# Kernel optimization log

Measured on AMD Instinct MI355X. Metric: run time of the kernel, lower is better.

Reference implementation:

```python
import jax, jax.numpy as jnp
import numpy as np
import math

# Hardcoded model constants (from source globals)
N_LAYERS = 4
MAX_SEQ_LEN = 34
VOCAB_SIZE = 14
TOK_DIM = 3
POS_DIM = 3
D_MODEL = 6
HEAD_DIM = 3
N_POS = 10
MAX_DIGITS = 10
ANSWER_LEN = 11
X_START, PLUS_POS, Y_START, EQ_POS, Z_START, EOS_POS = 0, 10, 11, 21, 22, 33
PLUS_TOKEN, EQUALS_TOKEN, EOS_TOKEN, PAD_TOKEN = 10, 11, 12, 13
BATCH = 16384


def _spiral(i, p):
    return (math.cos(2 * math.pi * i / p), math.sin(2 * math.pi * i / p), i / max(p - 1, 1))


def _build_pos_enc():
    pe = np.zeros((MAX_SEQ_LEN, POS_DIM), np.float32)
    for i in range(MAX_DIGITS):
        pe[X_START + i] = _spiral(i, N_POS)
    for i in range(MAX_DIGITS):
        pe[Y_START + i] = _spiral(i, N_POS)
    for i in range(min(ANSWER_LEN, N_POS)):
        pe[Z_START + i] = _spiral(i, N_POS)
    pe[Z_START + 10] = [0.0, 0.0, 1.5]
    pe[PLUS_POS] = [2.0, 0.0, -1.0]
    pe[EQ_POS] = [0.0, 2.0, -1.0]
    pe[EOS_POS] = [-2.0, 0.0, -1.0]
    return jnp.asarray(pe)


def _build_tok_emb():
    emb = np.zeros((VOCAB_SIZE, TOK_DIM), np.float32)
    for d in range(10):
        emb[d] = _spiral(d, 10)
    emb[PLUS_TOKEN] = [2.0, 0.0, -1.0]
    emb[EQUALS_TOKEN] = [0.0, 2.0, -1.0]
    emb[EOS_TOKEN] = [-2.0, 0.0, -1.0]
    emb[PAD_TOKEN] = [0.0, -2.0, -1.0]
    return jnp.asarray(emb)


def _xavier(key, shape):
    fan_out, fan_in = shape[-2], shape[-1]
    bound = math.sqrt(6.0 / (fan_in + fan_out))
    return jax.random.uniform(key, shape, jnp.float32, -bound, bound)


def setup_inputs() -> dict:
    key = jax.random.key(0)
    ks = jax.random.split(key, 10)
    L = N_LAYERS
    return {
        "idx": jax.random.randint(ks[0], (BATCH, MAX_SEQ_LEN), 0, VOCAB_SIZE),
        "tok_emb": _build_tok_emb(),
        "pos_enc": _build_pos_enc(),
        "ln_w": jnp.ones((L, D_MODEL), jnp.float32),
        "ln_b": jnp.zeros((L, D_MODEL), jnp.float32),
        "q1w": _xavier(ks[1], (L, HEAD_DIM, TOK_DIM)),
        "k1w": _xavier(ks[2], (L, HEAD_DIM, TOK_DIM)),
        "v1w": _xavier(ks[3], (L, HEAD_DIM, TOK_DIM)),
        "q2w": _xavier(ks[4], (L, HEAD_DIM, POS_DIM)),
        "k2w": _xavier(ks[5], (L, HEAD_DIM, POS_DIM)),
        "v2w": _xavier(ks[6], (L, HEAD_DIM, POS_DIM)),
        "out_w": _xavier(ks[7], (L, D_MODEL, 2 * HEAD_DIM)),
        "lnf_w": jnp.ones((D_MODEL,), jnp.float32),
        "lnf_b": jnp.zeros((D_MODEL,), jnp.float32),
        "head_w": _xavier(ks[8], (VOCAB_SIZE, D_MODEL)),
    }


def _layernorm(x, w, b, eps=1e-5):
    m = jnp.mean(x, -1, keepdims=True)
    v = jnp.mean(jnp.square(x - m), -1, keepdims=True)
    return (x - m) * jax.lax.rsqrt(v + eps) * w + b


def _attend(q, k, v, mask):
    # q,k,v: [B,T,HEAD_DIM]; mask: [T,T] bool lower-triangular
    s = jnp.einsum('bqd,bkd->bqk', q, k) / math.sqrt(HEAD_DIM)
    s = jnp.where(mask, s, jnp.finfo(s.dtype).min)
    return jnp.einsum('bqk,bkd->bqd', jax.nn.softmax(s, axis=-1), v)


def reference(idx, tok_emb, pos_enc, ln_w, ln_b, q1w, k1w, v1w, q2w, k2w, v2w, out_w, lnf_w, lnf_b, head_w):
    B, T = idx.shape
    tok = tok_emb[idx]                                   # [B,T,3]
    pos = jnp.broadcast_to(pos_enc[:T], (B, T, POS_DIM))  # [B,T,3]
    x = jnp.concatenate([tok, pos], axis=-1)             # [B,T,6]
    mask = jnp.tril(jnp.ones((T, T), bool))
    for l in range(N_LAYERS):
        h = _layernorm(x, ln_w[l], ln_b[l])
        ht, hp = h[..., :TOK_DIM], h[..., TOK_DIM:]
        o1 = _attend(ht @ q1w[l].T, ht @ k1w[l].T, ht @ v1w[l].T, mask)
        o2 = _attend(hp @ q2w[l].T, hp @ k2w[l].T, hp @ v2w[l].T, mask)
        x = x + jnp.concatenate([o1, o2], axis=-1) @ out_w[l].T
    x = _layernorm(x, lnf_w, lnf_b)
    return x @ head_w.T                                  # [B,T,VOCAB]
```

## Files before the change

kernel.cpp:

```cpp
#include <hip/hip_runtime.h>
#include <math.h>

#define N_LAYERS 4
#define SEQ      34
#define BATCH_N  16384
#define NE       16
#define NSLOT    16
#define VOCAB    14
#define QSCALE   0.8329806647638704f

__global__ __launch_bounds__(256) void addtrans_kernel(
    const int*   __restrict__ idx,
    const float* __restrict__ tok_emb,
    const float* __restrict__ pos_enc,
    const float* __restrict__ ln_w,
    const float* __restrict__ ln_b,
    const float* __restrict__ q1w,
    const float* __restrict__ k1w,
    const float* __restrict__ v1w,
    const float* __restrict__ q2w,
    const float* __restrict__ k2w,
    const float* __restrict__ v2w,
    const float* __restrict__ out_w,
    const float* __restrict__ lnf_w,
    const float* __restrict__ lnf_b,
    const float* __restrict__ head_w,
    float* __restrict__ out)
{
    __shared__ float4 kvs[3 * SEQ + 1][NE];

    const int x = threadIdx.x;
    const int y = threadIdx.y;
    const int b = (int)blockIdx.x * NE + x;

    int tp[3];
    tp[0] = y;
    tp[1] = 33 - y;
    tp[2] = (y < 2) ? (16 + y) : SEQ;

    float xs[3][6];
    #pragma unroll
    for (int p = 0; p < 3; ++p) {
        const int t = tp[p];
        if (t < SEQ) {
            const int tok = idx[(size_t)b * SEQ + t];
            xs[p][0] = tok_emb[tok * 3 + 0];
            xs[p][1] = tok_emb[tok * 3 + 1];
            xs[p][2] = tok_emb[tok * 3 + 2];
            xs[p][3] = pos_enc[t * 3 + 0];
            xs[p][4] = pos_enc[t * 3 + 1];
            xs[p][5] = pos_enc[t * 3 + 2];
        }
    }

    float qs[3][6];

    for (int l = 0; l < N_LAYERS; ++l) {
        __syncthreads();

        #pragma unroll
        for (int p = 0; p < 3; ++p) {
            const int t = tp[p];
            if (t < SEQ) {
                float h[6];
                {
                    const float* v = xs[p];
                    float m = (v[0]+v[1]+v[2]+v[3]+v[4]+v[5]) * (1.0f/6.0f);
                    float var = 0.f;
                    #pragma unroll
                    for (int i = 0; i < 6; ++i) { float d = v[i]-m; var += d*d; }
                    var *= (1.0f/6.0f);
                    float r = rsqrtf(var + 1e-5f);
                    #pragma unroll
                    for (int i = 0; i < 6; ++i)
                        h[i] = (v[i]-m) * r * ln_w[l*6+i] + ln_b[l*6+i];
                }
                float kk[6], vv[6];
                #pragma unroll
                for (int i = 0; i < 3; ++i) {
                    const int w = l*9 + i*3;
                    qs[p][i]   = (q1w[w]*h[0] + q1w[w+1]*h[1] + q1w[w+2]*h[2]) * QSCALE;
                    kk[i]      =  k1w[w]*h[0] + k1w[w+1]*h[1] + k1w[w+2]*h[2];
                    vv[i]      =  v1w[w]*h[0] + v1w[w+1]*h[1] + v1w[w+2]*h[2];
                    qs[p][3+i] = (q2w[w]*h[3] + q2w[w+1]*h[4] + q2w[w+2]*h[5]) * QSCALE;
                    kk[3+i]    =  k2w[w]*h[3] + k2w[w+1]*h[4] + k2w[w+2]*h[5];
                    vv[3+i]    =  v2w[w]*h[3] + v2w[w+1]*h[4] + v2w[w+2]*h[5];
                }
                kvs[0*SEQ + t][x] = make_float4(kk[0], kk[1], kk[2], kk[3]);
                kvs[1*SEQ + t][x] = make_float4(kk[4], kk[5], vv[0], vv[1]);
                kvs[2*SEQ + t][x] = make_float4(vv[2], vv[3], vv[4], vv[5]);
            }
        }
        __syncthreads();

        #pragma unroll
        for (int p = 0; p < 3; ++p) {
            const int t = tp[p];
            if (t < SEQ) {
                const float q0 = qs[p][0], q1 = qs[p][1], q2 = qs[p][2];
                const float q3 = qs[p][3], q4 = qs[p][4], q5 = qs[p][5];
                float l1 = 0.f, l2 = 0.f;
                float a0 = 0.f, a1 = 0.f, a2 = 0.f, a3 = 0.f, a4 = 0.f, a5 = 0.f;
                float4 c0 = kvs[0][x], c1 = kvs[SEQ][x], c2 = kvs[2*SEQ][x];
                for (int j = 0; j <= t; ++j) {
                    float4 n0 = kvs[j + 1][x];
                    float4 n1 = kvs[SEQ + j + 1][x];
                    float4 n2 = kvs[2*SEQ + j + 1][x];
                    float s1 = q0*c0.x + q1*c0.y + q2*c0.z;
                    float s2 = q3*c0.w + q4*c1.x + q5*c1.y;
                    float p1 = __builtin_amdgcn_exp2f(s1);
                    float p2 = __builtin_amdgcn_exp2f(s2);
                    l1 += p1;        l2 += p2;
                    a0 += p1*c1.z;   a1 += p1*c1.w;   a2 += p1*c2.x;
                    a3 += p2*c2.y;   a4 += p2*c2.z;   a5 += p2*c2.w;
                    c0 = n0; c1 = n1; c2 = n2;
                }
                const float i1 = __builtin_amdgcn_rcpf(l1);
                const float i2 = __builtin_amdgcn_rcpf(l2);
                float o[6] = { a0*i1, a1*i1, a2*i1, a3*i2, a4*i2, a5*i2 };
                #pragma unroll
                for (int i = 0; i < 6; ++i) {
                    const int w = l*36 + i*6;
                    xs[p][i] += out_w[w+0]*o[0] + out_w[w+1]*o[1] + out_w[w+2]*o[2]
                              + out_w[w+3]*o[3] + out_w[w+4]*o[4] + out_w[w+5]*o[5];
                }
            }
        }
    }

    #pragma unroll
    for (int p = 0; p < 3; ++p) {
        const int t = tp[p];
        if (t < SEQ) {
            float hf[6];
            {
                const float* v = xs[p];
                float m = (v[0]+v[1]+v[2]+v[3]+v[4]+v[5]) * (1.0f/6.0f);
                float var = 0.f;
                #pragma unroll
                for (int i = 0; i < 6; ++i) { float d = v[i]-m; var += d*d; }
                var *= (1.0f/6.0f);
                float r = rsqrtf(var + 1e-5f);
                #pragma unroll
                for (int i = 0; i < 6; ++i)
                    hf[i] = (v[i]-m) * r * lnf_w[i] + lnf_b[i];
            }
            float lg[VOCAB];
            #pragma unroll
            for (int c = 0; c < VOCAB; ++c) {
                const int w = c*6;
                lg[c] = head_w[w+0]*hf[0] + head_w[w+1]*hf[1] + head_w[w+2]*hf[2]
                      + head_w[w+3]*hf[3] + head_w[w+4]*hf[4] + head_w[w+5]*hf[5];
            }
            float2* op = (float2*)(out + ((size_t)b * SEQ + t) * VOCAB);
            #pragma unroll
            for (int c = 0; c < 7; ++c)
                op[c] = make_float2(lg[2*c], lg[2*c+1]);
        }
    }
}

extern "C" void kernel_launch(void* const* d_in, const int* in_sizes, int n_in,
                              void* d_out, int out_size, void* d_ws, size_t ws_size,
                              hipStream_t stream) {
    const int*   idx     = (const int*)  d_in[0];
    const float* tok_emb = (const float*)d_in[1];
    const float* pos_enc = (const float*)d_in[2];
    const float* ln_w    = (const float*)d_in[3];
    const float* ln_b    = (const float*)d_in[4];
    const float* q1w     = (const float*)d_in[5];
    const float* k1w     = (const float*)d_in[6];
    const float* v1w     = (const float*)d_in[7];
    const float* q2w     = (const float*)d_in[8];
    const float* k2w     = (const float*)d_in[9];
    const float* v2w     = (const float*)d_in[10];
    const float* out_w   = (const float*)d_in[11];
    const float* lnf_w   = (const float*)d_in[12];
    const float* lnf_b   = (const float*)d_in[13];
    const float* head_w  = (const float*)d_in[14];
    float* out = (float*)d_out;

    dim3 block(NE, NSLOT);
    const int grid = BATCH_N / NE;
    addtrans_kernel<<<grid, block, 0, stream>>>(
        idx, tok_emb, pos_enc, ln_w, ln_b,
        q1w, k1w, v1w, q2w, k2w, v2w,
        out_w, lnf_w, lnf_b, head_w, out);
}
```

Before: 148.6 us.

## Fuse per-thread query positions into one shared KV sweep with 128-thread blocks

Each thread now owns up to five query positions (8 slots per batch element instead of 16). The attention loop reads each K/V row from LDS once and applies it to every owned query, predicated by the causal bound, rather than running a separate loop per position. This cuts LDS traffic and loop overhead and balances work across slots. The cost is more registers per thread, predicated iterations that do no useful work, and half as many threads per block.

```diff
diff --git a/kernel.cpp b/kernel.cpp
--- a/kernel.cpp
+++ b/kernel.cpp
@@ -5,11 +5,12 @@
 #define SEQ      34
 #define BATCH_N  16384
 #define NE       16
-#define NSLOT    16
+#define NSLOT    8
+#define NT       5
 #define VOCAB    14
 #define QSCALE   0.8329806647638704f
 
-__global__ __launch_bounds__(256) void addtrans_kernel(
+__global__ __launch_bounds__(128) void addtrans_kernel(
     const int*   __restrict__ idx,
     const float* __restrict__ tok_emb,
     const float* __restrict__ pos_enc,
@@ -29,42 +30,45 @@
 {
     __shared__ float4 kvs[3 * SEQ + 1][NE];
 
-    const int x = threadIdx.x;
-    const int y = threadIdx.y;
+    const int x = threadIdx.x & (NE - 1);
+    const int y = threadIdx.x >> 4;
     const int b = (int)blockIdx.x * NE + x;
 
-    int tp[3];
-    tp[0] = y;
-    tp[1] = 33 - y;
-    tp[2] = (y < 2) ? (16 + y) : SEQ;
-
-    float xs[3][6];
+    int tp[NT];
+    tp[0] = (y < 2) ? (32 + y) : (24 + y);
+    tp[1] = y;
+    tp[2] = 8 + y;
+    tp[3] = 16 + y;
+    tp[4] = (y < 2) ? (24 + y) : -1;
+    const int jmax = tp[0];
+
+    float xs[NT][6];
     #pragma unroll
-    for (int p = 0; p < 3; ++p) {
-        const int t = tp[p];
-        if (t < SEQ) {
+    for (int k = 0; k < NT; ++k) {
+        const int t = tp[k];
+        if (t >= 0) {
             const int tok = idx[(size_t)b * SEQ + t];
-            xs[p][0] = tok_emb[tok * 3 + 0];
-            xs[p][1] = tok_emb[tok * 3 + 1];
-            xs[p][2] = tok_emb[tok * 3 + 2];
-            xs[p][3] = pos_enc[t * 3 + 0];
-            xs[p][4] = pos_enc[t * 3 + 1];
-            xs[p][5] = pos_enc[t * 3 + 2];
+            xs[k][0] = tok_emb[tok * 3 + 0];
+            xs[k][1] = tok_emb[tok * 3 + 1];
+            xs[k][2] = tok_emb[tok * 3 + 2];
+            xs[k][3] = pos_enc[t * 3 + 0];
+            xs[k][4] = pos_enc[t * 3 + 1];
+            xs[k][5] = pos_enc[t * 3 + 2];
         }
     }
 
-    float qs[3][6];
+    float qs[NT][6];
 
     for (int l = 0; l < N_LAYERS; ++l) {
         __syncthreads();
 
         #pragma unroll
-        for (int p = 0; p < 3; ++p) {
-            const int t = tp[p];
-            if (t < SEQ) {
+        for (int k = 0; k < NT; ++k) {
+            const int t = tp[k];
+            if (t >= 0) {
                 float h[6];
                 {
-                    const float* v = xs[p];
+                    const float* v = xs[k];
                     float m = (v[0]+v[1]+v[2]+v[3]+v[4]+v[5]) * (1.0f/6.0f);
                     float var = 0.f;
                     #pragma unroll
@@ -79,10 +83,10 @@
                 #pragma unroll
                 for (int i = 0; i < 3; ++i) {
                     const int w = l*9 + i*3;
-                    qs[p][i]   = (q1w[w]*h[0] + q1w[w+1]*h[1] + q1w[w+2]*h[2]) * QSCALE;
+                    qs[k][i]   = (q1w[w]*h[0] + q1w[w+1]*h[1] + q1w[w+2]*h[2]) * QSCALE;
                     kk[i]      =  k1w[w]*h[0] + k1w[w+1]*h[1] + k1w[w+2]*h[2];
                     vv[i]      =  v1w[w]*h[0] + v1w[w+1]*h[1] + v1w[w+2]*h[2];
-                    qs[p][3+i] = (q2w[w]*h[3] + q2w[w+1]*h[4] + q2w[w+2]*h[5]) * QSCALE;
+                    qs[k][3+i] = (q2w[w]*h[3] + q2w[w+1]*h[4] + q2w[w+2]*h[5]) * QSCALE;
                     kk[3+i]    =  k2w[w]*h[3] + k2w[w+1]*h[4] + k2w[w+2]*h[5];
                     vv[3+i]    =  v2w[w]*h[3] + v2w[w+1]*h[4] + v2w[w+2]*h[5];
                 }
@@ -93,35 +97,45 @@
         }
         __syncthreads();
 
+        float l1[NT], l2[NT], a[NT][6];
         #pragma unroll
-        for (int p = 0; p < 3; ++p) {
-            const int t = tp[p];
-            if (t < SEQ) {
-                const float q0 = qs[p][0], q1 = qs[p][1], q2 = qs[p][2];
-                const float q3 = qs[p][3], q4 = qs[p][4], q5 = qs[p][5];
-                float l1 = 0.f, l2 = 0.f;
-                float a0 = 0.f, a1 = 0.f, a2 = 0.f, a3 = 0.f, a4 = 0.f, a5 = 0.f;
-                float4 c0 = kvs[0][x], c1 = kvs[SEQ][x], c2 = kvs[2*SEQ][x];
-                for (int j = 0; j <= t; ++j) {
-                    float4 n0 = kvs[j + 1][x];
-                    float4 n1 = kvs[SEQ + j + 1][x];
-                    float4 n2 = kvs[2*SEQ + j + 1][x];
-                    float s1 = q0*c0.x + q1*c0.y + q2*c0.z;
-                    float s2 = q3*c0.w + q4*c1.x + q5*c1.y;
+        for (int k = 0; k < NT; ++k) {
+            l1[k] = 0.f; l2[k] = 0.f;
+            #pragma unroll
+            for (int i = 0; i < 6; ++i) a[k][i] = 0.f;
+        }
+        float4 c0 = kvs[0][x], c1 = kvs[SEQ][x], c2 = kvs[2*SEQ][x];
+        #pragma unroll 2
+        for (int j = 0; j <= jmax; ++j) {
+            float4 n0 = kvs[j + 1][x];
+            float4 n1 = kvs[SEQ + j + 1][x];
+            float4 n2 = kvs[2*SEQ + j + 1][x];
+            #pragma unroll
+            for (int k = 0; k < NT; ++k) {
+                if (k == 0 || j <= tp[k]) {
+                    float s1 = qs[k][0]*c0.x + qs[k][1]*c0.y + qs[k][2]*c0.z;
+                    float s2 = qs[k][3]*c0.w + qs[k][4]*c1.x + qs[k][5]*c1.y;
                     float p1 = __builtin_amdgcn_exp2f(s1);
                     float p2 = __builtin_amdgcn_exp2f(s2);
-                    l1 += p1;        l2 += p2;
-                    a0 += p1*c1.z;   a1 += p1*c1.w;   a2 += p1*c2.x;
-                    a3 += p2*c2.y;   a4 += p2*c2.z;   a5 += p2*c2.w;
-                    c0 = n0; c1 = n1; c2 = n2;
-                }
-                const float i1 = __builtin_amdgcn_rcpf(l1);
-                const float i2 = __builtin_amdgcn_rcpf(l2);
-                float o[6] = { a0*i1, a1*i1, a2*i1, a3*i2, a4*i2, a5*i2 };
+                    l1[k] += p1;        l2[k] += p2;
+                    a[k][0] += p1*c1.z; a[k][1] += p1*c1.w; a[k][2] += p1*c2.x;
+                    a[k][3] += p2*c2.y; a[k][4] += p2*c2.z; a[k][5] += p2*c2.w;
+                }
+            }
+            c0 = n0; c1 = n1; c2 = n2;
+        }
+
+        #pragma unroll
+        for (int k = 0; k < NT; ++k) {
+            if (tp[k] >= 0) {
+                const float i1 = __builtin_amdgcn_rcpf(l1[k]);
+                const float i2 = __builtin_amdgcn_rcpf(l2[k]);
+                float o[6] = { a[k][0]*i1, a[k][1]*i1, a[k][2]*i1,
+                               a[k][3]*i2, a[k][4]*i2, a[k][5]*i2 };
                 #pragma unroll
                 for (int i = 0; i < 6; ++i) {
                     const int w = l*36 + i*6;
-                    xs[p][i] += out_w[w+0]*o[0] + out_w[w+1]*o[1] + out_w[w+2]*o[2]
+                    xs[k][i] += out_w[w+0]*o[0] + out_w[w+1]*o[1] + out_w[w+2]*o[2]
                               + out_w[w+3]*o[3] + out_w[w+4]*o[4] + out_w[w+5]*o[5];
                 }
             }
@@ -129,12 +143,12 @@
     }
 
     #pragma unroll
-    for (int p = 0; p < 3; ++p) {
-        const int t = tp[p];
-        if (t < SEQ) {
+    for (int k = 0; k < NT; ++k) {
+        const int t = tp[k];
+        if (t >= 0) {
             float hf[6];
             {
-                const float* v = xs[p];
+                const float* v = xs[k];
                 float m = (v[0]+v[1]+v[2]+v[3]+v[4]+v[5]) * (1.0f/6.0f);
                 float var = 0.f;
                 #pragma unroll
@@ -180,9 +194,8 @@
     const float* head_w  = (const float*)d_in[14];
     float* out = (float*)d_out;
 
-    dim3 block(NE, NSLOT);
     const int grid = BATCH_N / NE;
-    addtrans_kernel<<<grid, block, 0, stream>>>(
+    addtrans_kernel<<<grid, NE * NSLOT, 0, stream>>>(
         idx, tok_emb, pos_enc, ln_w, ln_b,
         q1w, k1w, v1w, q2w, k2w, v2w,
         out_w, lnf_w, lnf_b, head_w, out);
```

New measurement: 146.2 us. About the same (-1.6%).
